# Kernel tuning notes

Measured on AMD Instinct MI355X. Metric: run time of the kernel, lower is better.

The kernel has to match this reference:

```python
import jax, jax.numpy as jnp
import numpy as np
import math

HIDDEN = 512
BATCH, SEQ = 4, 4096


def setup_inputs() -> dict:
    key = jax.random.key(0)
    ks = jax.random.split(key, 7)
    s = 1.0 / math.sqrt(HIDDEN)
    return {
        "X": jax.random.normal(ks[0], (BATCH, SEQ, HIDDEN), dtype=jnp.float32),
        "Wq": jax.random.uniform(ks[1], (HIDDEN, HIDDEN), jnp.float32, -s, s),
        "bq": jax.random.uniform(ks[2], (HIDDEN,), jnp.float32, -s, s),
        "Wk": jax.random.uniform(ks[3], (HIDDEN, HIDDEN), jnp.float32, -s, s),
        "bk": jax.random.uniform(ks[4], (HIDDEN,), jnp.float32, -s, s),
        "Wv": jax.random.uniform(ks[5], (HIDDEN, HIDDEN), jnp.float32, -s, s),
        "bv": jax.random.uniform(ks[6], (HIDDEN,), jnp.float32, -s, s),
    }


def reference(X, Wq, bq, Wk, bk, Wv, bv):
    # Q, K, V projections (torch Linear: y = x @ W.T + b; here W stored as [in, out])
    Q = jnp.einsum("bsd,de->bse", X, Wq) + bq
    K = jnp.einsum("bsd,de->bse", X, Wk) + bk
    V = jnp.einsum("bsd,de->bse", X, Wv) + bv
    scale = 1.0 / math.sqrt(Q.shape[-1])
    scores = jnp.einsum("bqd,bkd->bqk", Q, K) * scale  # [B, S, S]
    weights = jax.nn.softmax(scores, axis=-1)
    return jnp.einsum("bqk,bkd->bqd", weights, V)
```

## Files before the change

kernel.cpp:

```cpp
#include <hip/hip_runtime.h>
#include <hip/hip_bf16.h>
#include <math.h>


typedef __bf16 bfx8 __attribute__((ext_vector_type(8)));
typedef __bf16 bfx4 __attribute__((ext_vector_type(4)));
typedef float  fx4  __attribute__((ext_vector_type(4)));

#define HID   512
#define NBATCH 4
#define SEQ   4096
#define MROWS (NBATCH * SEQ)

#if __has_builtin(__builtin_amdgcn_exp2f)
#define EXPFN(x) __builtin_amdgcn_exp2f(x)
#define QSCALE 0.06375871589f
#else
#define EXPFN(x) __expf(x)
#define QSCALE 0.04419417382f
#endif

constexpr int MODE_QKV = 0;
constexpr int MODE_EXP = 2;
constexpr int MODE_DIV = 3;

__device__ __forceinline__ void gload_lds16(const __bf16* gsrc, __bf16* ldst) {
  __builtin_amdgcn_global_load_lds(
      (const __attribute__((address_space(1))) unsigned int*)gsrc,
      (__attribute__((address_space(3))) unsigned int*)ldst,
      16, 0, 0);
}

__global__ void prep_x_kernel(const float* __restrict__ X, __bf16* __restrict__ Xb) {
  int i = (blockIdx.x * 256 + threadIdx.x) * 4;
  const float4 v = *(const float4*)(X + i);
  bfx4 o;
  o[0] = (__bf16)v.x; o[1] = (__bf16)v.y; o[2] = (__bf16)v.z; o[3] = (__bf16)v.w;
  *(bfx4*)(Xb + i) = o;
}

__global__ void prep_w_kernel(const float* __restrict__ Wq, const float* __restrict__ Wk,
                              const float* __restrict__ Wv, __bf16* __restrict__ Wt) {
  int id  = blockIdx.x * 256 + threadIdx.x;
  int g   = id >> 18;
  int rem = id & ((1 << 18) - 1);
  int i   = rem >> 9;
  int o   = rem & 511;
  const float* W = (g == 0) ? Wq : ((g == 1) ? Wk : Wv);
  Wt[(g << 18) + (o << 9) + i] = (__bf16)W[rem];
}

template <int MODE, int TM, int TN>
__global__ __launch_bounds__(256)
void gemm_bt(const __bf16* __restrict__ A, const __bf16* __restrict__ B,
             void* __restrict__ C0v, void* __restrict__ C1v, void* __restrict__ C2v,
             const float* __restrict__ b0, const float* __restrict__ b1,
             const float* __restrict__ b2, float* __restrict__ rowsum,
             int lda, int ldb, int ldc, int K_,
             long sA, long sB, long sC, int sR) {
  constexpr int MT = TM / 32;
  constexpr int NT = TN / 32;
  constexpr int ABE = (TM + TN) * 64;
  constexpr int CTE = (MODE == MODE_DIV) ? TM * TN * 2 : TM * TN;
  constexpr int LDSN = (ABE > CTE) ? ABE : CTE;
  __shared__ __bf16 L[LDSN];
  __bf16* As = L;
  __bf16* Bs = L + TM * 64;

  const int z = blockIdx.z;
  A += (long)z * sA;
  B += (long)z * sB;

  const int tid  = threadIdx.x;
  const int lane = tid & 63;
  const int w    = tid >> 6;
  const int wm   = w >> 1, wn = w & 1;
  const int lm   = lane & 15, lq = lane >> 4;

  const int row0 = blockIdx.y * TM;
  const int col0 = blockIdx.x * TN;

  const __bf16* Ag = A + (long)row0 * lda;
  const __bf16* Bg = B + (long)col0 * ldb;

  fx4 acc[MT][NT] = {};

  for (int kt = 0; kt < K_; kt += 64) {
    __syncthreads();
#pragma unroll
    for (int it = 0; it < TM / 32; ++it) {
      int s = it * 256 + tid;
      int r = s >> 3, c = ((s & 7) ^ (r & 7)) << 3;
      gload_lds16(Ag + (long)r * lda + kt + c, As + it * 2048 + w * 512);
    }
#pragma unroll
    for (int it = 0; it < TN / 32; ++it) {
      int s = it * 256 + tid;
      int r = s >> 3, c = ((s & 7) ^ (r & 7)) << 3;
      gload_lds16(Bg + (long)r * ldb + kt + c, Bs + it * 2048 + w * 512);
    }
    __syncthreads();
#pragma unroll
    for (int kk = 0; kk < 2; ++kk) {
      bfx8 af[MT], bfr[NT];
#pragma unroll
      for (int t = 0; t < MT; ++t) {
        int ra = wm * (TM / 2) + t * 16 + lm;
        af[t] = *(const bfx8*)(As + ra * 64 + (((kk * 4 + lq) ^ (ra & 7)) << 3));
      }
#pragma unroll
      for (int t = 0; t < NT; ++t) {
        int rb = wn * (TN / 2) + t * 16 + lm;
        bfr[t] = *(const bfx8*)(Bs + rb * 64 + (((kk * 4 + lq) ^ (rb & 7)) << 3));
      }
#pragma unroll
      for (int mt = 0; mt < MT; ++mt)
#pragma unroll
        for (int nt = 0; nt < NT; ++nt)
          acc[mt][nt] = __builtin_amdgcn_mfma_f32_16x16x32_bf16(af[mt], bfr[nt],
                                                                acc[mt][nt], 0, 0, 0);
    }
  }

  const int lr0 = wm * (TM / 2);
  const int lc0 = wn * (TN / 2);

  __syncthreads();

  if constexpr (MODE == MODE_QKV) {
    const int g   = col0 >> 9;
    const int gc  = col0 & 511;
    const float* bias = (g == 0) ? b0 : ((g == 1) ? b1 : b2);
    float bvv[NT];
#pragma unroll
    for (int nt = 0; nt < NT; ++nt) bvv[nt] = bias[gc + lc0 + nt * 16 + lm];

    if (g < 2) {
      __bf16* Ct = L;
#pragma unroll
      for (int mt = 0; mt < MT; ++mt)
#pragma unroll
        for (int nt = 0; nt < NT; ++nt)
#pragma unroll
          for (int i = 0; i < 4; ++i) {
            float v = acc[mt][nt][i] + bvv[nt];
            if (g == 0) v *= QSCALE;
            Ct[(lr0 + mt * 16 + lq * 4 + i) * TN + lc0 + nt * 16 + lm] = (__bf16)v;
          }
      __syncthreads();
      __bf16* C = (g == 0) ? (__bf16*)C0v : (__bf16*)C1v;
#pragma unroll
      for (int j = 0; j < TM * TN / 2048; ++j) {
        int s = j * 256 + tid;
        int off = s * 8;
        int r = off / TN, c = off % TN;
        *(bfx8*)(C + (long)(row0 + r) * ldc + gc + c) = *(const bfx8*)(Ct + off);
      }
    } else {
      __bf16* C = (__bf16*)C2v;
#pragma unroll
      for (int mt = 0; mt < MT; ++mt)
#pragma unroll
        for (int nt = 0; nt < NT; ++nt) {
          int c  = gc + lc0 + nt * 16 + lm;
          int rb = row0 + lr0 + mt * 16 + lq * 4;
          int b  = rb >> 12;
          int s  = rb & 4095;
          bfx4 pk;
#pragma unroll
          for (int i = 0; i < 4; ++i) pk[i] = (__bf16)(acc[mt][nt][i] + bvv[nt]);
          *(bfx4*)(C + ((long)b * HID + c) * SEQ + s) = pk;
        }
    }
  } else if constexpr (MODE == MODE_EXP) {
    __bf16* Ct = L;
    float* rsump = rowsum + (long)z * sR;
#pragma unroll
    for (int mt = 0; mt < MT; ++mt)
#pragma unroll
      for (int i = 0; i < 4; ++i) {
        int rl = lr0 + mt * 16 + lq * 4 + i;
        float rs = 0.f;
#pragma unroll
        for (int nt = 0; nt < NT; ++nt) {
          float e = EXPFN(acc[mt][nt][i]);
          Ct[rl * TN + lc0 + nt * 16 + lm] = (__bf16)e;
          rs += e;
        }
        rs += __shfl_xor(rs, 1);
        rs += __shfl_xor(rs, 2);
        rs += __shfl_xor(rs, 4);
        rs += __shfl_xor(rs, 8);
        if (lm == 0) atomicAdd(&rsump[row0 + rl], rs);
      }
    __syncthreads();
    __bf16* C = ((__bf16*)C0v) + (long)z * sC;
#pragma unroll
    for (int j = 0; j < TM * TN / 2048; ++j) {
      int s = j * 256 + tid;
      int off = s * 8;
      int r = off / TN, c = off % TN;
      *(bfx8*)(C + (long)(row0 + r) * ldc + col0 + c) = *(const bfx8*)(Ct + off);
    }
  } else {
    float* Cf = (float*)L;
    const float* rsump = rowsum + (long)z * sR;
#pragma unroll
    for (int mt = 0; mt < MT; ++mt)
#pragma unroll
      for (int i = 0; i < 4; ++i) {
        int rl = lr0 + mt * 16 + lq * 4 + i;
        float inv = 1.f / rsump[row0 + rl];
#pragma unroll
        for (int nt = 0; nt < NT; ++nt)
          Cf[rl * TN + lc0 + nt * 16 + lm] = acc[mt][nt][i] * inv;
      }
    __syncthreads();
    float* C = ((float*)C0v) + (long)z * sC;
#pragma unroll
    for (int j = 0; j < TM * TN / 1024; ++j) {
      int s = j * 256 + tid;
      int off = s * 4;
      int r = off / TN, c = off % TN;
      *(float4*)(C + (long)(row0 + r) * ldc + col0 + c) = *(const float4*)(Cf + off);
    }
  }
}

#define QK_STEP(CUR, NXT, DS, LOAD)                                          \
    {                                                                        \
      _Pragma("unroll")                                                      \
      for (int nt = 0; nt < 4; ++nt)                                         \
        if (LOAD) NXT[nt] = *(const bfx8*)(kp + (long)nt * (16 * HID) +      \
                                           ((DS) + 1) * 32);                 \
      __builtin_amdgcn_s_setprio(1);                                         \
      _Pragma("unroll")                                                      \
      for (int mt = 0; mt < 4; ++mt) {                                       \
        const int r = mt * 16 + lm;                                          \
        bfx8 af = *(const bfx8*)(Qs + r * 512 + (((DS) >> 1) << 6) +         \
                   ((((((DS) & 1) << 2) + lq) ^ (r & 7)) << 3));             \
        _Pragma("unroll")                                                    \
        for (int nt = 0; nt < 4; ++nt)                                       \
          s4[mt][nt] = __builtin_amdgcn_mfma_f32_16x16x32_bf16(af, CUR[nt],  \
                         s4[mt][nt], 0, 0, 0);                               \
      }                                                                      \
      __builtin_amdgcn_s_setprio(0);                                         \
    }

#define PV_STEP(CUR, NXT, KS, LOAD)                                          \
    {                                                                        \
      _Pragma("unroll")                                                      \
      for (int nt = 0; nt < 4; ++nt)                                         \
        if (LOAD) NXT[nt] = *(const bfx8*)(vp + (long)nt * (16 * SEQ) +      \
                                           ((KS) + 1) * 32);                 \
      __builtin_amdgcn_s_setprio(1);                                         \
      _Pragma("unroll")                                                      \
      for (int mt = 0; mt < 4; ++mt) {                                       \
        const int r = mt * 16 + lm;                                          \
        bfx8 pa = *(const bfx8*)(Ps + r * 512 +                              \
                   ((((KS) * 4 + lq) ^ (r & 7)) << 3));                      \
        _Pragma("unroll")                                                    \
        for (int nt = 0; nt < 4; ++nt)                                       \
          o[mt][nt] = __builtin_amdgcn_mfma_f32_16x16x32_bf16(pa, CUR[nt],   \
                        o[mt][nt], 0, 0, 0);                                 \
      }                                                                      \
      __builtin_amdgcn_s_setprio(0);                                         \
    }

__global__ __launch_bounds__(512, 2)
void flash_attn(const __bf16* __restrict__ Qg_, const __bf16* __restrict__ Kg_,
                const __bf16* __restrict__ Vg_, float* __restrict__ Og_) {
  __shared__ __bf16 Qs[64 * 512];
  __shared__ __bf16 Ps[64 * 512];
  __shared__ float  rsw[8 * 64];

  const int tid  = threadIdx.x;
  const int lane = tid & 63;
  const int w    = tid >> 6;
  const int lm   = lane & 15;
  const int lq   = lane >> 4;

  const int bid = blockIdx.x;
  const int z   = (bid & 7) >> 1;
  const int qb  = ((bid & 1) << 5) | (bid >> 3);
  const long q0 = (long)qb * 64;

  const __bf16* Qg = Qg_ + ((long)z * SEQ + q0) * HID;
  const __bf16* Kg = Kg_ + (long)z * SEQ * HID;
  const __bf16* Vg = Vg_ + (long)z * HID * SEQ;
  float*        Og = Og_ + ((long)z * SEQ + q0) * HID;

#pragma unroll
  for (int it = 0; it < 8; ++it) {
    int idx = it * 512 + tid;
    int r   = idx >> 6;
    int c6  = idx & 63;
    int src = (c6 & ~7) | ((c6 ^ r) & 7);
    gload_lds16(Qg + (long)r * HID + src * 8, Qs + (it * 512 + w * 64) * 8);
  }

  fx4 o[4][4]  = {};
  fx4 rs4[4]   = {};

  const __bf16* kp = Kg + (long)(w * 64 + lm) * HID + lq * 8;
  const __bf16* vp = Vg + (long)(w * 64 + lm) * SEQ + lq * 8;

  __syncthreads();

  for (int kt = 0; kt < 8; ++kt) {
    fx4 s4[4][4] = {};
    bfx8 bkA[4], bkB[4];
#pragma unroll
    for (int nt = 0; nt < 4; ++nt)
      bkA[nt] = *(const bfx8*)(kp + (long)nt * (16 * HID));
#pragma unroll
    for (int g = 0; g < 8; ++g) {
      QK_STEP(bkA, bkB, 2 * g, 1)
      QK_STEP(bkB, bkA, 2 * g + 1, (g < 7))
    }
    kp += (long)512 * HID;

    __syncthreads();

#pragma unroll
    for (int mt = 0; mt < 4; ++mt)
#pragma unroll
      for (int i = 0; i < 4; ++i) {
        const int r = mt * 16 + lq * 4 + i;
#pragma unroll
        for (int nt = 0; nt < 4; ++nt) {
          float e = EXPFN(s4[mt][nt][i]);
          rs4[mt][i] += e;
          const int c = w * 64 + nt * 16 + lm;
          Ps[r * 512 + ((((c >> 3) ^ (r & 7)) << 3) | (c & 7))] = (__bf16)e;
        }
      }
    __syncthreads();

    bfx8 bvA[4], bvB[4];
#pragma unroll
    for (int nt = 0; nt < 4; ++nt)
      bvA[nt] = *(const bfx8*)(vp + (long)nt * (16 * SEQ));
#pragma unroll
    for (int g = 0; g < 8; ++g) {
      PV_STEP(bvA, bvB, 2 * g, 1)
      PV_STEP(bvB, bvA, 2 * g + 1, (g < 7))
    }
    vp += 512;
  }

#pragma unroll
  for (int mt = 0; mt < 4; ++mt)
#pragma unroll
    for (int i = 0; i < 4; ++i) {
      float v = rs4[mt][i];
      v += __shfl_xor(v, 1);
      v += __shfl_xor(v, 2);
      v += __shfl_xor(v, 4);
      v += __shfl_xor(v, 8);
      if (lm == 0) rsw[w * 64 + mt * 16 + lq * 4 + i] = v;
    }
  __syncthreads();

#pragma unroll
  for (int mt = 0; mt < 4; ++mt)
#pragma unroll
    for (int i = 0; i < 4; ++i) {
      const int r = mt * 16 + lq * 4 + i;
      float t = rsw[r];
#pragma unroll
      for (int ww = 1; ww < 8; ++ww) t += rsw[ww * 64 + r];
      const float inv = 1.f / t;
#pragma unroll
      for (int nt = 0; nt < 4; ++nt)
        Og[(long)r * HID + w * 64 + nt * 16 + lm] = o[mt][nt][i] * inv;
    }
}

extern "C" void kernel_launch(void* const* d_in, const int* in_sizes, int n_in,
                              void* d_out, int out_size, void* d_ws, size_t ws_size,
                              hipStream_t stream) {
  (void)in_sizes; (void)n_in; (void)out_size; (void)ws_size;
  const float* X  = (const float*)d_in[0];
  const float* Wq = (const float*)d_in[1];
  const float* bq = (const float*)d_in[2];
  const float* Wk = (const float*)d_in[3];
  const float* bk = (const float*)d_in[4];
  const float* Wv = (const float*)d_in[5];
  const float* bv = (const float*)d_in[6];
  float* out = (float*)d_out;

  __bf16* Xb = (__bf16*)d_ws;
  __bf16* Wt = Xb + (long)MROWS * HID;
  __bf16* Q  = Wt + 3 * HID * HID;
  __bf16* Kb = Q + (long)MROWS * HID;
  __bf16* Vt = Kb + (long)MROWS * HID;

  prep_x_kernel<<<(MROWS * HID) / 1024, 256, 0, stream>>>(X, Xb);
  prep_w_kernel<<<(3 * HID * HID) / 256, 256, 0, stream>>>(Wq, Wk, Wv, Wt);

  gemm_bt<MODE_QKV, 128, 128><<<dim3(12, 128, 1), 256, 0, stream>>>(
      Xb, Wt, Q, Kb, Vt, bq, bk, bv, nullptr,
      HID, HID, HID, HID, 0, 0, 0, 0);

  flash_attn<<<dim3(256), 512, 0, stream>>>(Q, Kb, Vt, out);
}
```

Before: 397.2 us.

## Warp-specialize flash attention into QK/exp producers and PV consumers with double-buffered P

Splits the 8 waves into 4 producer waves that compute QK^T scores and exponentials for 256-key tiles, and 4 consumer waves that run the P·V MFMAs on the previous tile. P is double-buffered in LDS so the two stages overlap across iterations, which removes one barrier per tile. Exp pairs are packed with a DPP swap into 32-bit stores to halve the LDS write count. Register prefetch double-buffering of K and V is removed, and consumers now hold twice as many accumulators, so register pressure and load latency exposure may rise. The two stages may also be unbalanced in work.

```diff
diff --git a/kernel.cpp b/kernel.cpp
--- a/kernel.cpp
+++ b/kernel.cpp
@@ -227,58 +227,20 @@
   }
 }
 
-#define QK_STEP(CUR, NXT, DS, LOAD)                                          \
-    {                                                                        \
-      _Pragma("unroll")                                                      \
-      for (int nt = 0; nt < 4; ++nt)                                         \
-        if (LOAD) NXT[nt] = *(const bfx8*)(kp + (long)nt * (16 * HID) +      \
-                                           ((DS) + 1) * 32);                 \
-      __builtin_amdgcn_s_setprio(1);                                         \
-      _Pragma("unroll")                                                      \
-      for (int mt = 0; mt < 4; ++mt) {                                       \
-        const int r = mt * 16 + lm;                                          \
-        bfx8 af = *(const bfx8*)(Qs + r * 512 + (((DS) >> 1) << 6) +         \
-                   ((((((DS) & 1) << 2) + lq) ^ (r & 7)) << 3));             \
-        _Pragma("unroll")                                                    \
-        for (int nt = 0; nt < 4; ++nt)                                       \
-          s4[mt][nt] = __builtin_amdgcn_mfma_f32_16x16x32_bf16(af, CUR[nt],  \
-                         s4[mt][nt], 0, 0, 0);                               \
-      }                                                                      \
-      __builtin_amdgcn_s_setprio(0);                                         \
-    }
-
-#define PV_STEP(CUR, NXT, KS, LOAD)                                          \
-    {                                                                        \
-      _Pragma("unroll")                                                      \
-      for (int nt = 0; nt < 4; ++nt)                                         \
-        if (LOAD) NXT[nt] = *(const bfx8*)(vp + (long)nt * (16 * SEQ) +      \
-                                           ((KS) + 1) * 32);                 \
-      __builtin_amdgcn_s_setprio(1);                                         \
-      _Pragma("unroll")                                                      \
-      for (int mt = 0; mt < 4; ++mt) {                                       \
-        const int r = mt * 16 + lm;                                          \
-        bfx8 pa = *(const bfx8*)(Ps + r * 512 +                              \
-                   ((((KS) * 4 + lq) ^ (r & 7)) << 3));                      \
-        _Pragma("unroll")                                                    \
-        for (int nt = 0; nt < 4; ++nt)                                       \
-          o[mt][nt] = __builtin_amdgcn_mfma_f32_16x16x32_bf16(pa, CUR[nt],   \
-                        o[mt][nt], 0, 0, 0);                                 \
-      }                                                                      \
-      __builtin_amdgcn_s_setprio(0);                                         \
-    }
-
 __global__ __launch_bounds__(512, 2)
 void flash_attn(const __bf16* __restrict__ Qg_, const __bf16* __restrict__ Kg_,
                 const __bf16* __restrict__ Vg_, float* __restrict__ Og_) {
   __shared__ __bf16 Qs[64 * 512];
-  __shared__ __bf16 Ps[64 * 512];
-  __shared__ float  rsw[8 * 64];
+  __shared__ __bf16 Ps[2][64 * 256];
+  __shared__ float  rsw[4 * 64];
 
   const int tid  = threadIdx.x;
   const int lane = tid & 63;
   const int w    = tid >> 6;
   const int lm   = lane & 15;
   const int lq   = lane >> 4;
+  const bool prod = (w < 4);
+  const int p    = w & 3;
 
   const int bid = blockIdx.x;
   const int z   = (bid & 7) >> 1;
@@ -299,82 +261,114 @@
     gload_lds16(Qg + (long)r * HID + src * 8, Qs + (it * 512 + w * 64) * 8);
   }
 
-  fx4 o[4][4]  = {};
+  fx4 o[4][8]  = {};
   fx4 rs4[4]   = {};
 
-  const __bf16* kp = Kg + (long)(w * 64 + lm) * HID + lq * 8;
-  const __bf16* vp = Vg + (long)(w * 64 + lm) * SEQ + lq * 8;
+  const __bf16* kp = Kg + (long)(p * 64 + lm) * HID + lq * 8;
+  const __bf16* vp = Vg + (long)(p * 128 + lm) * SEQ + lq * 8;
 
   __syncthreads();
 
-  for (int kt = 0; kt < 8; ++kt) {
-    fx4 s4[4][4] = {};
-    bfx8 bkA[4], bkB[4];
-#pragma unroll
-    for (int nt = 0; nt < 4; ++nt)
-      bkA[nt] = *(const bfx8*)(kp + (long)nt * (16 * HID));
-#pragma unroll
-    for (int g = 0; g < 8; ++g) {
-      QK_STEP(bkA, bkB, 2 * g, 1)
-      QK_STEP(bkB, bkA, 2 * g + 1, (g < 7))
-    }
-    kp += (long)512 * HID;
-
+  for (int s = 0; s < 17; ++s) {
+    if (prod) {
+      if (s < 16) {
+        __bf16* Pb = Ps[s & 1];
+#pragma unroll
+        for (int h = 0; h < 2; ++h) {
+          fx4 s4[2][4] = {};
+#pragma unroll
+          for (int ds = 0; ds < 16; ++ds) {
+            bfx8 bk[4];
+#pragma unroll
+            for (int nt = 0; nt < 4; ++nt)
+              bk[nt] = *(const bfx8*)(kp + (long)nt * (16 * HID) + ds * 32);
+            __builtin_amdgcn_s_setprio(1);
+#pragma unroll
+            for (int mt = 0; mt < 2; ++mt) {
+              const int r = (h * 2 + mt) * 16 + lm;
+              bfx8 af = *(const bfx8*)(Qs + r * 512 + ((ds >> 1) << 6) +
+                         (((((ds & 1) << 2) + lq) ^ (r & 7)) << 3));
+#pragma unroll
+              for (int nt = 0; nt < 4; ++nt)
+                s4[mt][nt] = __builtin_amdgcn_mfma_f32_16x16x32_bf16(
+                                 af, bk[nt], s4[mt][nt], 0, 0, 0);
+            }
+            __builtin_amdgcn_s_setprio(0);
+          }
+#pragma unroll
+          for (int mt = 0; mt < 2; ++mt)
+#pragma unroll
+            for (int i = 0; i < 4; ++i) {
+              const int r = (h * 2 + mt) * 16 + lq * 4 + i;
+#pragma unroll
+              for (int nt = 0; nt < 4; ++nt) {
+                float e = EXPFN(s4[mt][nt][i]);
+                rs4[h * 2 + mt][i] += e;
+                float en = __uint_as_float((unsigned)__builtin_amdgcn_mov_dpp(
+                               (int)__float_as_uint(e), 0xB1, 0xF, 0xF, true));
+                if (!(lm & 1)) {
+                  const int c = p * 64 + nt * 16 + lm;
+                  union { __bf16 b[2]; unsigned u; } pk;
+                  pk.b[0] = (__bf16)e; pk.b[1] = (__bf16)en;
+                  *(unsigned*)(Pb + r * 256 +
+                      ((((c >> 3) ^ (r & 7)) << 3) | (c & 7))) = pk.u;
+                }
+              }
+            }
+        }
+        kp += 256 * (long)HID;
+      } else {
+#pragma unroll
+        for (int mt = 0; mt < 4; ++mt)
+#pragma unroll
+          for (int i = 0; i < 4; ++i) {
+            float v = rs4[mt][i];
+            v += __shfl_xor(v, 1);
+            v += __shfl_xor(v, 2);
+            v += __shfl_xor(v, 4);
+            v += __shfl_xor(v, 8);
+            if (lm == 0) rsw[p * 64 + mt * 16 + lq * 4 + i] = v;
+          }
+      }
+    } else if (s > 0) {
+      const __bf16* Pb = Ps[(s - 1) & 1];
+#pragma unroll
+      for (int ks = 0; ks < 8; ++ks) {
+        bfx8 bv[8];
+#pragma unroll
+        for (int nt = 0; nt < 8; ++nt)
+          bv[nt] = *(const bfx8*)(vp + (long)nt * (16 * SEQ) + ks * 32);
+        __builtin_amdgcn_s_setprio(1);
+#pragma unroll
+        for (int mt = 0; mt < 4; ++mt) {
+          const int r = mt * 16 + lm;
+          bfx8 pa = *(const bfx8*)(Pb + r * 256 +
+                     (((ks * 4 + lq) ^ (r & 7)) << 3));
+#pragma unroll
+          for (int nt = 0; nt < 8; ++nt)
+            o[mt][nt] = __builtin_amdgcn_mfma_f32_16x16x32_bf16(
+                            pa, bv[nt], o[mt][nt], 0, 0, 0);
+        }
+        __builtin_amdgcn_s_setprio(0);
+      }
+      vp += 256;
+    }
     __syncthreads();
-
+  }
+
+  if (!prod) {
 #pragma unroll
     for (int mt = 0; mt < 4; ++mt)
 #pragma unroll
       for (int i = 0; i < 4; ++i) {
         const int r = mt * 16 + lq * 4 + i;
-#pragma unroll
-        for (int nt = 0; nt < 4; ++nt) {
-          float e = EXPFN(s4[mt][nt][i]);
-          rs4[mt][i] += e;
-          const int c = w * 64 + nt * 16 + lm;
-          Ps[r * 512 + ((((c >> 3) ^ (r & 7)) << 3) | (c & 7))] = (__bf16)e;
-        }
-      }
-    __syncthreads();
-
-    bfx8 bvA[4], bvB[4];
-#pragma unroll
-    for (int nt = 0; nt < 4; ++nt)
-      bvA[nt] = *(const bfx8*)(vp + (long)nt * (16 * SEQ));
-#pragma unroll
-    for (int g = 0; g < 8; ++g) {
-      PV_STEP(bvA, bvB, 2 * g, 1)
-      PV_STEP(bvB, bvA, 2 * g + 1, (g < 7))
-    }
-    vp += 512;
+        float t = rsw[r] + rsw[64 + r] + rsw[128 + r] + rsw[192 + r];
+        const float inv = 1.f / t;
+#pragma unroll
+        for (int nt = 0; nt < 8; ++nt)
+          Og[(long)r * HID + p * 128 + nt * 16 + lm] = o[mt][nt][i] * inv;
+      }
   }
-
-#pragma unroll
-  for (int mt = 0; mt < 4; ++mt)
-#pragma unroll
-    for (int i = 0; i < 4; ++i) {
-      float v = rs4[mt][i];
-      v += __shfl_xor(v, 1);
-      v += __shfl_xor(v, 2);
-      v += __shfl_xor(v, 4);
-      v += __shfl_xor(v, 8);
-      if (lm == 0) rsw[w * 64 + mt * 16 + lq * 4 + i] = v;
-    }
-  __syncthreads();
-
-#pragma unroll
-  for (int mt = 0; mt < 4; ++mt)
-#pragma unroll
-    for (int i = 0; i < 4; ++i) {
-      const int r = mt * 16 + lq * 4 + i;
-      float t = rsw[r];
-#pragma unroll
-      for (int ww = 1; ww < 8; ++ww) t += rsw[ww * 64 + r];
-      const float inv = 1.f / t;
-#pragma unroll
-      for (int nt = 0; nt < 4; ++nt)
-        Og[(long)r * HID + w * 64 + nt * 16 + lm] = o[mt][nt][i] * inv;
-    }
 }
 
 extern "C" void kernel_launch(void* const* d_in, const int* in_sizes, int n_in,
```

Result: slower. 726.5 us (+82.9%).

## Halve attention query tile to 32 rows and double grid size

Applied to the files above, without the earlier changes.

The flash attention kernel now handles 32 query rows per block instead of 64, so the grid grows from 256 to 512 blocks and fills the GPU better. Per-block LDS and registers shrink, and the min-blocks launch bound is dropped. The P tile is written as packed bf16 pairs using a DPP lane swap, and the barrier moves from before the exp stage to after the PV stage. Each block still streams the full K and V for its batch, so global and L2 traffic for K/V roughly doubles.

```diff
diff --git a/kernel.cpp b/kernel.cpp
--- a/kernel.cpp
+++ b/kernel.cpp
@@ -11,6 +11,7 @@
 #define NBATCH 4
 #define SEQ   4096
 #define MROWS (NBATCH * SEQ)
+#define QROWS 32
 
 #if __has_builtin(__builtin_amdgcn_exp2f)
 #define EXPFN(x) __builtin_amdgcn_exp2f(x)
@@ -235,7 +236,7 @@
                                            ((DS) + 1) * 32);                 \
       __builtin_amdgcn_s_setprio(1);                                         \
       _Pragma("unroll")                                                      \
-      for (int mt = 0; mt < 4; ++mt) {                                       \
+      for (int mt = 0; mt < 2; ++mt) {                                       \
         const int r = mt * 16 + lm;                                          \
         bfx8 af = *(const bfx8*)(Qs + r * 512 + (((DS) >> 1) << 6) +         \
                    ((((((DS) & 1) << 2) + lq) ^ (r & 7)) << 3));             \
@@ -255,7 +256,7 @@
                                            ((KS) + 1) * 32);                 \
       __builtin_amdgcn_s_setprio(1);                                         \
       _Pragma("unroll")                                                      \
-      for (int mt = 0; mt < 4; ++mt) {                                       \
+      for (int mt = 0; mt < 2; ++mt) {                                       \
         const int r = mt * 16 + lm;                                          \
         bfx8 pa = *(const bfx8*)(Ps + r * 512 +                              \
                    ((((KS) * 4 + lq) ^ (r & 7)) << 3));                      \
@@ -267,12 +268,12 @@
       __builtin_amdgcn_s_setprio(0);                                         \
     }
 
-__global__ __launch_bounds__(512, 2)
+__global__ __launch_bounds__(512)
 void flash_attn(const __bf16* __restrict__ Qg_, const __bf16* __restrict__ Kg_,
                 const __bf16* __restrict__ Vg_, float* __restrict__ Og_) {
-  __shared__ __bf16 Qs[64 * 512];
-  __shared__ __bf16 Ps[64 * 512];
-  __shared__ float  rsw[8 * 64];
+  __shared__ __bf16 Qs[QROWS * 512];
+  __shared__ __bf16 Ps[QROWS * 512];
+  __shared__ float  rsw[8 * QROWS];
 
   const int tid  = threadIdx.x;
   const int lane = tid & 63;
@@ -281,9 +282,10 @@
   const int lq   = lane >> 4;
 
   const int bid = blockIdx.x;
-  const int z   = (bid & 7) >> 1;
-  const int qb  = ((bid & 1) << 5) | (bid >> 3);
-  const long q0 = (long)qb * 64;
+  const int x   = bid & 7;
+  const int z   = x >> 1;
+  const int qb  = ((x & 1) << 6) | (bid >> 3);
+  const long q0 = (long)qb * QROWS;
 
   const __bf16* Qg = Qg_ + ((long)z * SEQ + q0) * HID;
   const __bf16* Kg = Kg_ + (long)z * SEQ * HID;
@@ -291,7 +293,7 @@
   float*        Og = Og_ + ((long)z * SEQ + q0) * HID;
 
 #pragma unroll
-  for (int it = 0; it < 8; ++it) {
+  for (int it = 0; it < 4; ++it) {
     int idx = it * 512 + tid;
     int r   = idx >> 6;
     int c6  = idx & 63;
@@ -299,8 +301,8 @@
     gload_lds16(Qg + (long)r * HID + src * 8, Qs + (it * 512 + w * 64) * 8);
   }
 
-  fx4 o[4][4]  = {};
-  fx4 rs4[4]   = {};
+  fx4 o[2][4]  = {};
+  fx4 rs4[2]   = {};
 
   const __bf16* kp = Kg + (long)(w * 64 + lm) * HID + lq * 8;
   const __bf16* vp = Vg + (long)(w * 64 + lm) * SEQ + lq * 8;
@@ -308,22 +310,22 @@
   __syncthreads();
 
   for (int kt = 0; kt < 8; ++kt) {
-    fx4 s4[4][4] = {};
-    bfx8 bkA[4], bkB[4];
-#pragma unroll
-    for (int nt = 0; nt < 4; ++nt)
-      bkA[nt] = *(const bfx8*)(kp + (long)nt * (16 * HID));
-#pragma unroll
-    for (int g = 0; g < 8; ++g) {
-      QK_STEP(bkA, bkB, 2 * g, 1)
-      QK_STEP(bkB, bkA, 2 * g + 1, (g < 7))
+    fx4 s4[2][4] = {};
+    {
+      bfx8 bkA[4], bkB[4];
+#pragma unroll
+      for (int nt = 0; nt < 4; ++nt)
+        bkA[nt] = *(const bfx8*)(kp + (long)nt * (16 * HID));
+#pragma unroll
+      for (int g = 0; g < 8; ++g) {
+        QK_STEP(bkA, bkB, 2 * g, 1)
+        QK_STEP(bkB, bkA, 2 * g + 1, (g < 7))
+      }
     }
     kp += (long)512 * HID;
 
-    __syncthreads();
-
-#pragma unroll
-    for (int mt = 0; mt < 4; ++mt)
+#pragma unroll
+    for (int mt = 0; mt < 2; ++mt)
 #pragma unroll
       for (int i = 0; i < 4; ++i) {
         const int r = mt * 16 + lq * 4 + i;
@@ -331,26 +333,36 @@
         for (int nt = 0; nt < 4; ++nt) {
           float e = EXPFN(s4[mt][nt][i]);
           rs4[mt][i] += e;
-          const int c = w * 64 + nt * 16 + lm;
-          Ps[r * 512 + ((((c >> 3) ^ (r & 7)) << 3) | (c & 7))] = (__bf16)e;
+          float en = __uint_as_float((unsigned)__builtin_amdgcn_mov_dpp(
+                         (int)__float_as_uint(e), 0xB1, 0xF, 0xF, true));
+          if (!(lm & 1)) {
+            const int c = w * 64 + nt * 16 + lm;
+            union { __bf16 b[2]; unsigned u; } pk;
+            pk.b[0] = (__bf16)e; pk.b[1] = (__bf16)en;
+            *(unsigned*)(Ps + r * 512 +
+                ((((c >> 3) ^ (r & 7)) << 3) | (c & 7))) = pk.u;
+          }
         }
       }
     __syncthreads();
 
-    bfx8 bvA[4], bvB[4];
-#pragma unroll
-    for (int nt = 0; nt < 4; ++nt)
-      bvA[nt] = *(const bfx8*)(vp + (long)nt * (16 * SEQ));
-#pragma unroll
-    for (int g = 0; g < 8; ++g) {
-      PV_STEP(bvA, bvB, 2 * g, 1)
-      PV_STEP(bvB, bvA, 2 * g + 1, (g < 7))
+    {
+      bfx8 bvA[4], bvB[4];
+#pragma unroll
+      for (int nt = 0; nt < 4; ++nt)
+        bvA[nt] = *(const bfx8*)(vp + (long)nt * (16 * SEQ));
+#pragma unroll
+      for (int g = 0; g < 8; ++g) {
+        PV_STEP(bvA, bvB, 2 * g, 1)
+        PV_STEP(bvB, bvA, 2 * g + 1, (g < 7))
+      }
     }
     vp += 512;
+    __syncthreads();
   }
 
 #pragma unroll
-  for (int mt = 0; mt < 4; ++mt)
+  for (int mt = 0; mt < 2; ++mt)
 #pragma unroll
     for (int i = 0; i < 4; ++i) {
       float v = rs4[mt][i];
@@ -358,18 +370,18 @@
       v += __shfl_xor(v, 2);
       v += __shfl_xor(v, 4);
       v += __shfl_xor(v, 8);
-      if (lm == 0) rsw[w * 64 + mt * 16 + lq * 4 + i] = v;
+      if (lm == 0) rsw[w * QROWS + mt * 16 + lq * 4 + i] = v;
     }
   __syncthreads();
 
 #pragma unroll
-  for (int mt = 0; mt < 4; ++mt)
+  for (int mt = 0; mt < 2; ++mt)
 #pragma unroll
     for (int i = 0; i < 4; ++i) {
       const int r = mt * 16 + lq * 4 + i;
       float t = rsw[r];
 #pragma unroll
-      for (int ww = 1; ww < 8; ++ww) t += rsw[ww * 64 + r];
+      for (int ww = 1; ww < 8; ++ww) t += rsw[ww * QROWS + r];
       const float inv = 1.f / t;
 #pragma unroll
       for (int nt = 0; nt < 4; ++nt)
@@ -403,5 +415,5 @@
       Xb, Wt, Q, Kb, Vt, bq, bk, bv, nullptr,
       HID, HID, HID, HID, 0, 0, 0, 0);
 
-  flash_attn<<<dim3(256), 512, 0, stream>>>(Q, Kb, Vt, out);
-}
+  flash_attn<<<dim3(512), 512, 0, stream>>>(Q, Kb, Vt, out);
+}
```

Measured after the change: 607.2 us. 1.53x slower.
